# Performance work log

Hardware: AMD Instinct MI355X
Metric: run time of the kernel (lower is better)

## Reference

```python
import jax, jax.numpy as jnp
import numpy as np

EPS = 1e-6
H = 8          # num_heads
GAMMA = 0.99   # fixed decay (requires_grad=False in source)
RPE_LAYERS = 3


def srms(x):
    # SimpleRMSNorm: x / (rms(x) + eps), rms = ||x||_2 / sqrt(d) = sqrt(mean(x^2))
    return x / (jnp.sqrt(jnp.mean(x * x, axis=-1, keepdims=True)) + EPS)


def setup_inputs() -> dict:
    key = jax.random.key(0)
    B, N, E = 8, 2048, 512
    D1 = 1536            # int(3*512) // 8 * 8
    R = 512              # rpe_embedding
    ks = jax.random.split(key, 12)

    def lin(k, i, o):
        return jax.random.normal(k, (i, o), jnp.float32) * (i ** -0.5)

    x = jax.random.normal(ks[0], (B, N, E), jnp.float32)
    return {
        "x": x,
        "Wu": lin(ks[1], E, D1), "bu": jnp.zeros((D1,), jnp.float32),
        "Wv": lin(ks[2], E, D1), "bv": jnp.zeros((D1,), jnp.float32),
        "Wo": lin(ks[3], D1, E), "bo": jnp.zeros((E,), jnp.float32),
        "rpe_Win": lin(ks[4], 1, R), "rpe_bin": jnp.zeros((R,), jnp.float32),
        "rpe_W": jax.random.normal(ks[5], (RPE_LAYERS, R, R), jnp.float32) * (R ** -0.5),
        "rpe_b": jnp.zeros((RPE_LAYERS, R), jnp.float32),
        "rpe_Wout": lin(ks[6], R, D1), "rpe_bout": jnp.zeros((D1,), jnp.float32),
    }


def reference(x, Wu, bu, Wv, bv, Wo, bo, rpe_Win, rpe_bin, rpe_W, rpe_b, rpe_Wout, rpe_bout):
    B, N, E = x.shape
    u = jax.nn.silu(x @ Wu + bu)                     # b n d1
    v = jax.nn.silu(x @ Wv + bv)                     # b n d1
    D1 = v.shape[-1]
    D = D1 // H
    v = v.reshape(B, N, H, D).transpose(0, 2, 1, 3)  # b h n d

    # RPE MLP over positions: row 0 is the zero index, rows 1..N-1 are pos indices 1..N-1 (par_type=1)
    idx = jnp.arange(0, N, dtype=x.dtype)[:, None]   # (N, 1)
    h = idx @ rpe_Win + rpe_bin                      # (N, R)
    for i in range(RPE_LAYERS):                      # residual=False
        h = jax.nn.relu(srms(h)) @ rpe_W[i] + rpe_b[i]
    coeffs = jax.nn.relu(srms(h)) @ rpe_Wout + rpe_bout   # (N, H*D)
    coeffs = coeffs.reshape(N, H, D).transpose(1, 0, 2)   # h n d

    zero = coeffs[:, :1]                             # h 1 d  (a_0)
    pos = coeffs[:, 1:]                              # h n-1 d (a_1..a_{n-1})
    decay = GAMMA ** jnp.arange(1, N, dtype=x.dtype)[None, :, None]
    pos = pos * decay
    # causal: a = [a0, a1..a_{n-1}, a0]; act_type='none' -> identity
    a = jnp.concatenate([zero, pos, zero], axis=1)   # h, n+1, d

    # Toeplitz mixing via circular convolution of length 2n (torch.fft.rfft/irfft, norm='backward')
    m = 2 * N
    yf = jnp.fft.rfft(v, m, axis=2)                  # b h m/2+1 d (complex)
    af = jnp.fft.rfft(a, m, axis=1)[None]            # 1 h m/2+1 d
    out = jnp.fft.irfft(yf * af, m, axis=2)[:, :, :N, :]  # b h n d

    out = out.transpose(0, 2, 1, 3).reshape(B, N, D1)     # b n (h d)
    out = u * out
    return out @ Wo + bo
```

## Files before the change

### kernel.cpp

```cpp
#include <hip/hip_runtime.h>
#include <cstdint>


typedef unsigned short ushort_t;
typedef __attribute__((ext_vector_type(8))) short short8;
typedef __attribute__((ext_vector_type(4))) float f32x4;

#define AS1 __attribute__((address_space(1)))
#define AS3 __attribute__((address_space(3)))

#define SW1(j) ((j) ^ (((j) >> 4) & 15))
#define SW2(j) ((j) ^ ((((j) >> 6) & 7) << 1))

__device__ __forceinline__ float bf2f(ushort_t b) {
  union { unsigned u; float f; } x; x.u = ((unsigned)b) << 16; return x.f;
}
__device__ __forceinline__ ushort_t f2bf(float f) {
  union { float f; unsigned u; } x; x.f = f;
  unsigned r = x.u + 0x7fffu + ((x.u >> 16) & 1u);
  return (ushort_t)(r >> 16);
}

__device__ __forceinline__ void gload_lds16(const void* g, void* l) {
  auto gp = reinterpret_cast<const AS1 unsigned*>(reinterpret_cast<uintptr_t>(g));
  auto lp = reinterpret_cast<AS3 unsigned*>(reinterpret_cast<uintptr_t>(l));
  __builtin_amdgcn_global_load_lds(gp, lp, 16, 0, 0);
}

template<int MODE>
__launch_bounds__(256, 2)
__global__ void gemm_bt(const ushort_t* __restrict__ A, const ushort_t* __restrict__ Bt,
                        const float* __restrict__ bias, void* __restrict__ Cout,
                        void* __restrict__ Cout2, int M, int N, int K, float lng)
{
  __shared__ ushort_t As[128 * 64];
  __shared__ ushort_t Bs[128 * 64];
  const int tid  = threadIdx.x;
  const int wave = tid >> 6, lane = tid & 63;
  const int nb = N >> 7;
  const int bm = (int)blockIdx.x / nb, bn = (int)blockIdx.x % nb;
  const int m0 = bm << 7, n0 = bn << 7;
  const int lrow = lane & 15, quad = lane >> 4;
  const int wm = (wave >> 1) << 6, wn = (wave & 1) << 6;
  const int srow = lane >> 3;
  const int scol = (lane & 7) << 3;

  f32x4 acc[4][4] = {};

  for (int kt = 0; kt < K; kt += 64) {
    __syncthreads();
#pragma unroll
    for (int i = 0; i < 4; ++i) {
      const int ci  = i * 4 + wave;
      const int row = ci * 8 + srow;
      gload_lds16(A  + (long)(m0 + row) * K + kt + scol, (void*)&As[ci * 512]);
      gload_lds16(Bt + (long)(n0 + row) * K + kt + scol, (void*)&Bs[ci * 512]);
    }
    __syncthreads();
#pragma unroll
    for (int s = 0; s < 2; ++s) {
      short8 afr[4], bfr[4];
#pragma unroll
      for (int i = 0; i < 4; ++i)
        afr[i] = *(const short8*)&As[(wm + i * 16 + lrow) * 64 + s * 32 + quad * 8];
#pragma unroll
      for (int j = 0; j < 4; ++j)
        bfr[j] = *(const short8*)&Bs[(wn + j * 16 + lrow) * 64 + s * 32 + quad * 8];
#pragma unroll
      for (int i = 0; i < 4; ++i)
#pragma unroll
        for (int j = 0; j < 4; ++j)
          acc[i][j] = __builtin_amdgcn_mfma_f32_16x16x32_bf16(afr[i], bfr[j], acc[i][j], 0, 0, 0);
    }
  }

#pragma unroll
  for (int i = 0; i < 4; ++i) {
    const int rowb = m0 + wm + i * 16 + quad * 4;
#pragma unroll
    for (int j = 0; j < 4; ++j) {
      const int col = n0 + wn + j * 16 + lrow;
      const float bv = bias[col];
      if (MODE == 0) {
#pragma unroll
        for (int r = 0; r < 4; ++r)
          ((float*)Cout)[(long)(rowb + r) * N + col] = acc[i][j][r] + bv;
      } else {
        if (col < 1536) {
#pragma unroll
          for (int r = 0; r < 4; ++r) {
            float val = acc[i][j][r] + bv;
            float sv = val / (1.f + __expf(-val));
            ((ushort_t*)Cout)[(long)(rowb + r) * 1536 + col] = f2bf(sv);
          }
        } else {
          union { ushort_t h[4]; uint2 u2; } pk;
#pragma unroll
          for (int r = 0; r < 4; ++r) {
            float val = acc[i][j][r] + bv;
            float sv = val / (1.f + __expf(-val));
            pk.h[r] = f2bf(sv);
          }
          *(uint2*)((ushort_t*)Cout2 + (long)(col - 1536) * 16384 + rowb) = pk.u2;
        }
      }
    }
  }
}

template<int MODE>
__launch_bounds__(256, 2)
__global__ void gemm64_bt(const ushort_t* __restrict__ A, const ushort_t* __restrict__ Bt,
                          const float* __restrict__ bias, float* __restrict__ Cout,
                          int M, int N, int K, float lng)
{
  __shared__ ushort_t As[64 * 64];
  __shared__ ushort_t Bs[64 * 64];
  const int tid = threadIdx.x, wave = tid >> 6, lane = tid & 63;
  const int nb = N >> 6;
  const int bm = (int)blockIdx.x / nb, bn = (int)blockIdx.x % nb;
  const int m0 = bm << 6, n0 = bn << 6;
  const int lrow = lane & 15, quad = lane >> 4;
  const int wm = (wave >> 1) << 5, wn = (wave & 1) << 5;
  const int srow = lane >> 3, scol = (lane & 7) << 3;

  f32x4 acc[2][2] = {};

  for (int kt = 0; kt < K; kt += 64) {
    __syncthreads();
#pragma unroll
    for (int i = 0; i < 2; ++i) {
      const int ci = i * 4 + wave;
      const int row = ci * 8 + srow;
      gload_lds16(A  + (long)(m0 + row) * K + kt + scol, (void*)&As[ci * 512]);
      gload_lds16(Bt + (long)(n0 + row) * K + kt + scol, (void*)&Bs[ci * 512]);
    }
    __syncthreads();
#pragma unroll
    for (int s = 0; s < 2; ++s) {
      short8 afr[2], bfr[2];
#pragma unroll
      for (int i = 0; i < 2; ++i)
        afr[i] = *(const short8*)&As[(wm + i * 16 + lrow) * 64 + s * 32 + quad * 8];
#pragma unroll
      for (int j = 0; j < 2; ++j)
        bfr[j] = *(const short8*)&Bs[(wn + j * 16 + lrow) * 64 + s * 32 + quad * 8];
#pragma unroll
      for (int i = 0; i < 2; ++i)
#pragma unroll
        for (int j = 0; j < 2; ++j)
          acc[i][j] = __builtin_amdgcn_mfma_f32_16x16x32_bf16(afr[i], bfr[j], acc[i][j], 0, 0, 0);
    }
  }

#pragma unroll
  for (int i = 0; i < 2; ++i) {
    const int rowb = m0 + wm + i * 16 + quad * 4;
#pragma unroll
    for (int j = 0; j < 2; ++j) {
      const int col = n0 + wn + j * 16 + lrow;
      const float bv = bias[col];
#pragma unroll
      for (int r = 0; r < 4; ++r) {
        const int row = rowb + r;
        float val = acc[i][j][r] + bv;
        if (MODE == 0) Cout[(long)row * N + col] = val;
        else           Cout[(long)col * M + row] = val * __expf(lng * (float)row);
      }
    }
  }
}

__device__ __forceinline__ void srms_relu_store(float v0, float v1, ushort_t* out,
                                                long rowbase, int tid)
{
  float ss = v0 * v0 + v1 * v1;
#pragma unroll
  for (int off = 32; off; off >>= 1) ss += __shfl_down(ss, off);
  __shared__ float ps[4];
  const int wave = tid >> 6, lane = tid & 63;
  if (lane == 0) ps[wave] = ss;
  __syncthreads();
  float tot = ps[0] + ps[1] + ps[2] + ps[3];
  float sc = 1.f / (sqrtf(tot * (1.f / 512.f)) + 1e-6f);
  out[rowbase + tid]       = f2bf(fmaxf(v0 * sc, 0.f));
  out[rowbase + tid + 256] = f2bf(fmaxf(v1 * sc, 0.f));
}

__launch_bounds__(256)
__global__ void rpe_norm(const float* __restrict__ h, ushort_t* __restrict__ out)
{
  const int n = blockIdx.x, tid = threadIdx.x;
  float v0 = h[(long)n * 512 + tid];
  float v1 = h[(long)n * 512 + tid + 256];
  srms_relu_store(v0, v1, out, (long)n * 512, tid);
}

__device__ __forceinline__ void wtrans_body(const float* __restrict__ src,
                                            ushort_t* __restrict__ dst,
                                            int K, int N, int lb, int tid,
                                            float (*tile)[33])
{
  const int nbx = N >> 5;
  const int bx = lb % nbx, by = lb / nbx;
  const int n0 = bx << 5, k0 = by << 5;
  const int tx = tid & 31, ty = tid >> 5;
  for (int yy = ty; yy < 32; yy += 8)
    tile[yy][tx] = src[(long)(k0 + yy) * N + n0 + tx];
  __syncthreads();
  for (int yy = ty; yy < 32; yy += 8)
    dst[(long)(n0 + yy) * K + k0 + tx] = f2bf(tile[tx][yy]);
}

__launch_bounds__(256)
__global__ void prep_all(const float* __restrict__ Wu, const float* __restrict__ Wv,
                         const float* __restrict__ Wo, const float* __restrict__ rW,
                         const float* __restrict__ rWout,
                         const float* __restrict__ bu, const float* __restrict__ bv,
                         const float* __restrict__ x,
                         const float* __restrict__ rWin, const float* __restrict__ rbin,
                         ushort_t* __restrict__ wuvt, ushort_t* __restrict__ wot,
                         ushort_t* __restrict__ wrt, ushort_t* __restrict__ wroutt,
                         float* __restrict__ buvb, ushort_t* __restrict__ xb,
                         float2* __restrict__ twg, float2* __restrict__ twh,
                         ushort_t* __restrict__ a0)
{
  __shared__ float tile[32][33];
  const int bid = blockIdx.x, tid = threadIdx.x;
  if (bid < 3840) {
    const float* src; ushort_t* dst; int K, N, lb;
    if (bid < 768)       { src = Wu;    dst = wuvt;              K = 512;  N = 1536; lb = bid; }
    else if (bid < 1536) { src = Wv;    dst = wuvt + 1536L*512;  K = 512;  N = 1536; lb = bid - 768; }
    else if (bid < 2304) { src = Wo;    dst = wot;               K = 1536; N = 512;  lb = bid - 1536; }
    else if (bid < 2560) { src = rW;              dst = wrt;              K = 512; N = 512; lb = bid - 2304; }
    else if (bid < 2816) { src = rW + 512L*512;   dst = wrt + 512L*512;   K = 512; N = 512; lb = bid - 2560; }
    else if (bid < 3072) { src = rW + 2L*512*512; dst = wrt + 2L*512*512; K = 512; N = 512; lb = bid - 2816; }
    else                 { src = rWout; dst = wroutt;            K = 512;  N = 1536; lb = bid - 3072; }
    wtrans_body(src, dst, K, N, lb, tid, tile);
  } else if (bid < 3846) {
    int i = (bid - 3840) * 256 + tid;
    if (i < 1536) { buvb[i] = bu[i]; buvb[1536 + i] = bv[i]; }
  } else if (bid < 12038) {
    long i = (long)(bid - 3846) * 1024 + tid * 4;
    float4 f = *(const float4*)(x + i);
    unsigned lo = (unsigned)f2bf(f.x) | ((unsigned)f2bf(f.y) << 16);
    unsigned hi = (unsigned)f2bf(f.z) | ((unsigned)f2bf(f.w) << 16);
    *(uint2*)(xb + i) = make_uint2(lo, hi);
  } else if (bid < 12046) {
    int j = (bid - 12038) * 256 + tid;
    float s, c;
    __sincosf((float)j * (6.283185307179586f / 2048.f), &s, &c);
    twg[j] = make_float2(c, -s);
    float s2, c2;
    __sincosf((float)j * (3.14159265358979f / 2048.f), &s2, &c2);
    twh[j] = make_float2(c2, -s2);
  } else {
    const int n = bid - 12046;
    const float fn = (float)n;
    float v0 = fn * rWin[tid] + rbin[tid];
    float v1 = fn * rWin[tid + 256] + rbin[tid + 256];
    srms_relu_store(v0, v1, a0, (long)n * 512, tid);
  }
}

__device__ __forceinline__ float2 cmulf(float2 a, float2 b) {
  return make_float2(a.x * b.x - a.y * b.y, a.x * b.y + a.y * b.x);
}
__device__ __forceinline__ float2 cadd(float2 a, float2 b){ return make_float2(a.x+b.x, a.y+b.y); }
__device__ __forceinline__ float2 csub(float2 a, float2 b){ return make_float2(a.x-b.x, a.y-b.y); }
__device__ __forceinline__ float2 cmni(float2 z){ return make_float2(z.y, -z.x); }
__device__ __forceinline__ float2 cw8(float2 z){
  const float s = 0.70710678118654752f;
  return make_float2(s*(z.x+z.y), s*(z.y-z.x));
}
__device__ __forceinline__ float2 cw83(float2 z){
  const float s = 0.70710678118654752f;
  return make_float2(s*(z.y-z.x), -s*(z.x+z.y));
}

__device__ __forceinline__ void dft8(const float2* u, float2* y)
{
  float2 a0=cadd(u[0],u[4]), a1=cadd(u[1],u[5]), a2=cadd(u[2],u[6]), a3=cadd(u[3],u[7]);
  float2 b0=csub(u[0],u[4]), b1=cw8(csub(u[1],u[5])), b2=cmni(csub(u[2],u[6])), b3=cw83(csub(u[3],u[7]));
  float2 c0=cadd(a0,a2), c1=csub(a0,a2), c2=cadd(a1,a3), c3=cmni(csub(a1,a3));
  y[0]=cadd(c0,c2); y[2]=cadd(c1,c3); y[4]=csub(c0,c2); y[6]=csub(c1,c3);
  float2 d0=cadd(b0,b2), d1=csub(b0,b2), d2=cadd(b1,b3), d3=cmni(csub(b1,b3));
  y[1]=cadd(d0,d2); y[3]=cadd(d1,d3); y[5]=csub(d0,d2); y[7]=csub(d1,d3);
}
__device__ __forceinline__ void dft8_hz(const float2* u, float2* y)
{
  float2 b1=cw8(u[1]), b2=cmni(u[2]), b3=cw83(u[3]);
  float2 c0=cadd(u[0],u[2]), c1=csub(u[0],u[2]), c2=cadd(u[1],u[3]), c3=cmni(csub(u[1],u[3]));
  y[0]=cadd(c0,c2); y[2]=cadd(c1,c3); y[4]=csub(c0,c2); y[6]=csub(c1,c3);
  float2 d0=cadd(u[0],b2), d1=csub(u[0],b2), d2=cadd(b1,b3), d3=cmni(csub(b1,b3));
  y[1]=cadd(d0,d2); y[3]=cadd(d1,d3); y[5]=csub(d0,d2); y[7]=csub(d1,d3);
}

template<bool HZ>
__device__ void fft2048_r8_2(float2* b0a, float2* b1a, float2* b0b, float2* b1b,
                             const float2* __restrict__ tw, int tid)
{
  float2 u[8], v[8], y[8], z[8];
  {
    const int i = tid;
#pragma unroll
    for (int m = 0; m < (HZ ? 4 : 8); ++m) { u[m] = b0a[i + 256*m]; v[m] = b0b[i + 256*m]; }
    if (HZ) { dft8_hz(u, y); dft8_hz(v, z); } else { dft8(u, y); dft8(v, z); }
    const int j = i << 3;
#pragma unroll
    for (int m = 0; m < 8; ++m) { b1a[SW1(j + m)] = y[m]; b1b[SW1(j + m)] = z[m]; }
  }
  __syncthreads();
  {
    const int i = tid, k = i & 7, tb = k << 5;
    float2 w[8];
#pragma unroll
    for (int m = 1; m < 8; ++m) w[m] = tw[m * tb];
#pragma unroll
    for (int m = 0; m < 8; ++m) { u[m] = b1a[SW1(i + 256*m)]; v[m] = b1b[SW1(i + 256*m)]; }
#pragma unroll
    for (int m = 1; m < 8; ++m) { u[m] = cmulf(u[m], w[m]); v[m] = cmulf(v[m], w[m]); }
    dft8(u, y); dft8(v, z);
    const int j = ((i - k) << 3) + k;
#pragma unroll
    for (int m = 0; m < 8; ++m) { b0a[SW2(j + 8*m)] = y[m]; b0b[SW2(j + 8*m)] = z[m]; }
  }
  __syncthreads();
  {
    const int i = tid, k = i & 63, tb = k << 2;
    float2 w[8];
#pragma unroll
    for (int m = 1; m < 8; ++m) w[m] = tw[m * tb];
#pragma unroll
    for (int m = 0; m < 8; ++m) { u[m] = b0a[SW2(i + 256*m)]; v[m] = b0b[SW2(i + 256*m)]; }
#pragma unroll
    for (int m = 1; m < 8; ++m) { u[m] = cmulf(u[m], w[m]); v[m] = cmulf(v[m], w[m]); }
    dft8(u, y); dft8(v, z);
    const int j = ((i - k) << 3) + k;
#pragma unroll
    for (int m = 0; m < 8; ++m) { b1a[j + 64*m] = y[m]; b1b[j + 64*m] = z[m]; }
  }
  __syncthreads();
#pragma unroll
  for (int hh = 0; hh < 2; ++hh) {
    const int i = tid + (hh << 8);
    float2 w1 = tw[i], w2 = tw[2 * i], w3 = tw[3 * i];
    float2 q0 = b1a[i], q1 = b1a[i + 512], q2 = b1a[i + 1024], q3 = b1a[i + 1536];
    float2 r0 = b1b[i], r1 = b1b[i + 512], r2 = b1b[i + 1024], r3 = b1b[i + 1536];
    q1 = cmulf(q1, w1); q2 = cmulf(q2, w2); q3 = cmulf(q3, w3);
    r1 = cmulf(r1, w1); r2 = cmulf(r2, w2); r3 = cmulf(r3, w3);
    {
      float2 v0 = cadd(q0, q2), v2 = csub(q0, q2);
      float2 v1 = cadd(q1, q3), v3 = cmni(csub(q1, q3));
      b0a[i]        = cadd(v0, v1);
      b0a[i + 512]  = cadd(v2, v3);
      b0a[i + 1024] = csub(v0, v1);
      b0a[i + 1536] = csub(v2, v3);
    }
    {
      float2 v0 = cadd(r0, r2), v2 = csub(r0, r2);
      float2 v1 = cadd(r1, r3), v3 = cmni(csub(r1, r3));
      b0b[i]        = cadd(v0, v1);
      b0b[i + 512]  = cadd(v2, v3);
      b0b[i + 1024] = csub(v0, v1);
      b0b[i + 1536] = csub(v2, v3);
    }
  }
  __syncthreads();
}

__launch_bounds__(256, 2)
__global__ void fft_kernel_spec(const float* __restrict__ kern, float2* __restrict__ af,
                                const float2* __restrict__ twg, const float2* __restrict__ twh)
{
  __shared__ float2 bx0[2048], by0[2048], bx1[2048], by1[2048];
  const int tid = threadIdx.x;
  const int c0 = (int)blockIdx.x * 2;
  const float* ka = kern + (long)c0 * 2048;
  const float* kb = ka + 2048;
  for (int j = tid; j < 1024; j += 256) {
    bx0[j] = *(const float2*)(ka + 2 * j);
    bx1[j] = *(const float2*)(kb + 2 * j);
  }
  __syncthreads();
  fft2048_r8_2<true>(bx0, by0, bx1, by1, twg, tid);
  float2* af0 = af + (long)c0 * 2052;
  float2* af1 = af0 + 2052;
  for (int k = tid; k <= 1024; k += 256) {
    const float2 W = twh[k];
    const int kn = (2048 - k) & 2047;
    {
      float2 Zk = bx0[k], Zn = bx0[kn];
      float2 E = make_float2(0.5f * (Zk.x + Zn.x), 0.5f * (Zk.y - Zn.y));
      float2 O = make_float2(0.5f * (Zk.y + Zn.y), 0.5f * (Zn.x - Zk.x));
      float2 WO = cmulf(W, O);
      af0[k] = make_float2(E.x + WO.x, E.y + WO.y);
      if (k != 0 && k != 1024) af0[2048 - k] = make_float2(E.x - WO.x, -(E.y - WO.y));
      if (k == 0)              af0[2048]     = make_float2(E.x - WO.x, -(E.y - WO.y));
    }
    {
      float2 Zk = bx1[k], Zn = bx1[kn];
      float2 E = make_float2(0.5f * (Zk.x + Zn.x), 0.5f * (Zk.y - Zn.y));
      float2 O = make_float2(0.5f * (Zk.y + Zn.y), 0.5f * (Zn.x - Zk.x));
      float2 WO = cmulf(W, O);
      af1[k] = make_float2(E.x + WO.x, E.y + WO.y);
      if (k != 0 && k != 1024) af1[2048 - k] = make_float2(E.x - WO.x, -(E.y - WO.y));
      if (k == 0)              af1[2048]     = make_float2(E.x - WO.x, -(E.y - WO.y));
    }
  }
}

__launch_bounds__(256, 2)
__global__ void fft_conv(ushort_t* __restrict__ vt, const float2* __restrict__ af,
                         const float2* __restrict__ twg, const float2* __restrict__ twh)
{
  __shared__ float2 bx0[2048], by0[2048], bx1[2048], by1[2048];
  const int tid = threadIdx.x;
  const long s0 = (long)blockIdx.x * 2;
  const int c = (int)(s0 >> 3);
  ushort_t* vsa = vt + s0 * 2048;
  ushort_t* vsb = vsa + 2048;
#pragma unroll
  for (int jj = 0; jj < 4; ++jj) {
    const int j = tid + jj * 256;
    unsigned pa = *(const unsigned*)(vsa + 2 * j);
    unsigned pb = *(const unsigned*)(vsb + 2 * j);
    bx0[j] = make_float2(bf2f((ushort_t)(pa & 0xffffu)), bf2f((ushort_t)(pa >> 16)));
    bx1[j] = make_float2(bf2f((ushort_t)(pb & 0xffffu)), bf2f((ushort_t)(pb >> 16)));
  }
  __syncthreads();
  fft2048_r8_2<true>(bx0, by0, bx1, by1, twg, tid);
  const float2* afc = af + (long)c * 2052;
  for (int k = tid; k <= 1024; k += 256) {
    const float2 A0 = afc[k], A1 = afc[2048 - k], W = twh[k];
    const float2 cW = make_float2(W.x, -W.y);
    const int kn = (2048 - k) & 2047;
    {
      float2 Zk = bx0[k], Zn = bx0[kn];
      float2 E = make_float2(0.5f * (Zk.x + Zn.x), 0.5f * (Zk.y - Zn.y));
      float2 O = make_float2(0.5f * (Zk.y + Zn.y), 0.5f * (Zn.x - Zk.x));
      float2 WO = cmulf(W, O);
      float2 Xk = make_float2(E.x + WO.x, E.y + WO.y);
      float2 Xn = make_float2(E.x - WO.x, -(E.y - WO.y));
      float2 Pk = cmulf(Xk, A0);
      float2 Pn = cmulf(Xn, A1);
      float2 E2 = make_float2(0.5f * (Pk.x + Pn.x), 0.5f * (Pk.y - Pn.y));
      float2 G  = make_float2(0.5f * (Pk.x - Pn.x), 0.5f * (Pk.y + Pn.y));
      float2 Fo = cmulf(cW, G);
      by0[k] = make_float2(E2.x - Fo.y, -(E2.y + Fo.x));
      if (k != 0 && k != 1024)
        by0[2048 - k] = make_float2(E2.x + Fo.y, E2.y - Fo.x);
    }
    {
      float2 Zk = bx1[k], Zn = bx1[kn];
      float2 E = make_float2(0.5f * (Zk.x + Zn.x), 0.5f * (Zk.y - Zn.y));
      float2 O = make_float2(0.5f * (Zk.y + Zn.y), 0.5f * (Zn.x - Zk.x));
      float2 WO = cmulf(W, O);
      float2 Xk = make_float2(E.x + WO.x, E.y + WO.y);
      float2 Xn = make_float2(E.x - WO.x, -(E.y - WO.y));
      float2 Pk = cmulf(Xk, A0);
      float2 Pn = cmulf(Xn, A1);
      float2 E2 = make_float2(0.5f * (Pk.x + Pn.x), 0.5f * (Pk.y - Pn.y));
      float2 G  = make_float2(0.5f * (Pk.x - Pn.x), 0.5f * (Pk.y + Pn.y));
      float2 Fo = cmulf(cW, G);
      by1[k] = make_float2(E2.x - Fo.y, -(E2.y + Fo.x));
      if (k != 0 && k != 1024)
        by1[2048 - k] = make_float2(E2.x + Fo.y, E2.y - Fo.x);
    }
  }
  __syncthreads();
  fft2048_r8_2<false>(by0, bx0, by1, bx1, twg, tid);
  const float inv = 1.f / 2048.f;
#pragma unroll
  for (int jj = 0; jj < 4; ++jj) {
    const int j = tid + jj * 256;
    float2 ra = by0[j], rb = by1[j];
    unsigned oa = (unsigned)f2bf(ra.x * inv) | ((unsigned)f2bf(-ra.y * inv) << 16);
    unsigned ob = (unsigned)f2bf(rb.x * inv) | ((unsigned)f2bf(-rb.y * inv) << 16);
    *(unsigned*)(vsa + 2 * j) = oa;
    *(unsigned*)(vsb + 2 * j) = ob;
  }
}

__launch_bounds__(256)
__global__ void gate_trans(const ushort_t* __restrict__ convt, ushort_t* __restrict__ u)
{
  __shared__ ushort_t tile[64][65];
  const int bc = (int)blockIdx.x % 24, br = (int)blockIdx.x / 24;
  const int c0 = bc << 6, r0 = br << 6;
  const int tx = threadIdx.x & 63, ty = threadIdx.x >> 6;
  for (int yy = ty; yy < 64; yy += 4)
    tile[yy][tx] = convt[(long)(c0 + yy) * 16384 + r0 + tx];
  __syncthreads();
  for (int yy = ty; yy < 64; yy += 4) {
    long ui = (long)(r0 + yy) * 1536 + c0 + tx;
    float uu = bf2f(u[ui]);
    float cc = bf2f(tile[tx][yy]);
    u[ui] = f2bf(uu * cc);
  }
}

extern "C" void kernel_launch(void* const* d_in, const int* in_sizes, int n_in,
                              void* d_out, int out_size, void* d_ws, size_t ws_size,
                              hipStream_t stream)
{
  const float* x     = (const float*)d_in[0];
  const float* Wu    = (const float*)d_in[1];
  const float* bu    = (const float*)d_in[2];
  const float* Wv    = (const float*)d_in[3];
  const float* bv    = (const float*)d_in[4];
  const float* Wo    = (const float*)d_in[5];
  const float* bo    = (const float*)d_in[6];
  const float* rWin  = (const float*)d_in[7];
  const float* rbin  = (const float*)d_in[8];
  const float* rW    = (const float*)d_in[9];
  const float* rb    = (const float*)d_in[10];
  const float* rWout = (const float*)d_in[11];
  const float* rbout = (const float*)d_in[12];

  char* base = (char*)d_ws;
  size_t off = 0;
  auto alloc = [&](size_t bytes) -> char* {
    size_t r = (off + 255) & ~(size_t)255; off = r + bytes; return base + r;
  };
  ushort_t* wuvt   = (ushort_t*)alloc(3072L * 512 * 2);
  ushort_t* wot    = (ushort_t*)alloc(512L * 1536 * 2);
  ushort_t* wrt    = (ushort_t*)alloc(3L * 512 * 512 * 2);
  ushort_t* wroutt = (ushort_t*)alloc(1536L * 512 * 2);
  float*    buvb   = (float*)   alloc(3072L * 4);
  ushort_t* a0     = (ushort_t*)alloc(2048L * 512 * 2);
  float2*   af     = (float2*)  alloc(1536L * 2052 * 8);
  float2*   twg    = (float2*)  alloc(2048L * 8);
  float2*   twh    = (float2*)  alloc(2048L * 8);
  char*     X      = alloc(16384L * 512 * 2);
  ushort_t* u      = (ushort_t*)alloc(16384L * 1536 * 2);
  ushort_t* vt     = (ushort_t*)alloc(1536L * 16384 * 2);
  ushort_t* xb   = (ushort_t*)X;
  float*    h    = (float*)X;
  float*    kern = (float*)(X + 4L * 1024 * 1024);

  const float lng = -0.01005033585350145f;

  prep_all<<<dim3(14094), dim3(256), 0, stream>>>(
      Wu, Wv, Wo, rW, rWout, bu, bv, x, rWin, rbin,
      wuvt, wot, wrt, wroutt, buvb, xb, twg, twh, a0);

  gemm_bt<3><<<dim3(3072), dim3(256), 0, stream>>>(xb, wuvt, buvb, u, vt,
                                                   16384, 3072, 512, 0.f);

  for (int i = 0; i < 3; ++i) {
    gemm64_bt<0><<<dim3(256), dim3(256), 0, stream>>>(a0, wrt + (long)i * 512 * 512,
                                                      rb + (long)i * 512, h,
                                                      2048, 512, 512, 0.f);
    rpe_norm<<<dim3(2048), dim3(256), 0, stream>>>(h, a0);
  }
  gemm64_bt<2><<<dim3(768), dim3(256), 0, stream>>>(a0, wroutt, rbout, kern,
                                                    2048, 1536, 512, lng);
  fft_kernel_spec<<<dim3(768), dim3(256), 0, stream>>>(kern, af, twg, twh);

  fft_conv<<<dim3(6144), dim3(256), 0, stream>>>(vt, af, twg, twh);
  gate_trans<<<dim3(6144), dim3(256), 0, stream>>>(vt, u);
  gemm_bt<0><<<dim3(512), dim3(256), 0, stream>>>(u, wot, bo, d_out, nullptr,
                                                  16384, 512, 1536, 0.f);
}
```

Baseline: 493.8 us.

## Make the 2048-point FFT in-place to halve LDS and double occupancy

Replaces the ping-pong shared-memory FFT, which used four 2048-entry float2 buffers, with an in-place variant that uses two buffers. A barrier is added after each stage's loads so results can be written back into the same buffer. The spectral multiply in the convolution kernel now also writes in place. The LDS cut lets launch bounds rise from 2 to 4 blocks per CU, aiming to hide LDS and global latency in the FFT kernels, at the cost of extra barriers and a tighter per-thread register budget that could cause spills.

```diff
diff --git a/kernel.cpp b/kernel.cpp
--- a/kernel.cpp
+++ b/kernel.cpp
@@ -297,18 +297,19 @@
 }
 
 template<bool HZ>
-__device__ void fft2048_r8_2(float2* b0a, float2* b1a, float2* b0b, float2* b1b,
-                             const float2* __restrict__ tw, int tid)
+__device__ void fft2048_ip2(float2* ba, float2* bb,
+                            const float2* __restrict__ tw, int tid)
 {
   float2 u[8], v[8], y[8], z[8];
   {
     const int i = tid;
 #pragma unroll
-    for (int m = 0; m < (HZ ? 4 : 8); ++m) { u[m] = b0a[i + 256*m]; v[m] = b0b[i + 256*m]; }
+    for (int m = 0; m < (HZ ? 4 : 8); ++m) { u[m] = ba[i + 256*m]; v[m] = bb[i + 256*m]; }
     if (HZ) { dft8_hz(u, y); dft8_hz(v, z); } else { dft8(u, y); dft8(v, z); }
+    __syncthreads();
     const int j = i << 3;
 #pragma unroll
-    for (int m = 0; m < 8; ++m) { b1a[SW1(j + m)] = y[m]; b1b[SW1(j + m)] = z[m]; }
+    for (int m = 0; m < 8; ++m) { ba[SW1(j + m)] = y[m]; bb[SW1(j + m)] = z[m]; }
   }
   __syncthreads();
   {
@@ -317,13 +318,14 @@
 #pragma unroll
     for (int m = 1; m < 8; ++m) w[m] = tw[m * tb];
 #pragma unroll
-    for (int m = 0; m < 8; ++m) { u[m] = b1a[SW1(i + 256*m)]; v[m] = b1b[SW1(i + 256*m)]; }
+    for (int m = 0; m < 8; ++m) { u[m] = ba[SW1(i + 256*m)]; v[m] = bb[SW1(i + 256*m)]; }
 #pragma unroll
     for (int m = 1; m < 8; ++m) { u[m] = cmulf(u[m], w[m]); v[m] = cmulf(v[m], w[m]); }
     dft8(u, y); dft8(v, z);
+    __syncthreads();
     const int j = ((i - k) << 3) + k;
 #pragma unroll
-    for (int m = 0; m < 8; ++m) { b0a[SW2(j + 8*m)] = y[m]; b0b[SW2(j + 8*m)] = z[m]; }
+    for (int m = 0; m < 8; ++m) { ba[SW2(j + 8*m)] = y[m]; bb[SW2(j + 8*m)] = z[m]; }
   }
   __syncthreads();
   {
@@ -332,48 +334,49 @@
 #pragma unroll
     for (int m = 1; m < 8; ++m) w[m] = tw[m * tb];
 #pragma unroll
-    for (int m = 0; m < 8; ++m) { u[m] = b0a[SW2(i + 256*m)]; v[m] = b0b[SW2(i + 256*m)]; }
+    for (int m = 0; m < 8; ++m) { u[m] = ba[SW2(i + 256*m)]; v[m] = bb[SW2(i + 256*m)]; }
 #pragma unroll
     for (int m = 1; m < 8; ++m) { u[m] = cmulf(u[m], w[m]); v[m] = cmulf(v[m], w[m]); }
     dft8(u, y); dft8(v, z);
+    __syncthreads();
     const int j = ((i - k) << 3) + k;
 #pragma unroll
-    for (int m = 0; m < 8; ++m) { b1a[j + 64*m] = y[m]; b1b[j + 64*m] = z[m]; }
+    for (int m = 0; m < 8; ++m) { ba[j + 64*m] = y[m]; bb[j + 64*m] = z[m]; }
   }
   __syncthreads();
 #pragma unroll
   for (int hh = 0; hh < 2; ++hh) {
     const int i = tid + (hh << 8);
     float2 w1 = tw[i], w2 = tw[2 * i], w3 = tw[3 * i];
-    float2 q0 = b1a[i], q1 = b1a[i + 512], q2 = b1a[i + 1024], q3 = b1a[i + 1536];
-    float2 r0 = b1b[i], r1 = b1b[i + 512], r2 = b1b[i + 1024], r3 = b1b[i + 1536];
+    float2 q0 = ba[i], q1 = ba[i + 512], q2 = ba[i + 1024], q3 = ba[i + 1536];
+    float2 r0 = bb[i], r1 = bb[i + 512], r2 = bb[i + 1024], r3 = bb[i + 1536];
     q1 = cmulf(q1, w1); q2 = cmulf(q2, w2); q3 = cmulf(q3, w3);
     r1 = cmulf(r1, w1); r2 = cmulf(r2, w2); r3 = cmulf(r3, w3);
     {
       float2 v0 = cadd(q0, q2), v2 = csub(q0, q2);
       float2 v1 = cadd(q1, q3), v3 = cmni(csub(q1, q3));
-      b0a[i]        = cadd(v0, v1);
-      b0a[i + 512]  = cadd(v2, v3);
-      b0a[i + 1024] = csub(v0, v1);
-      b0a[i + 1536] = csub(v2, v3);
+      ba[i]        = cadd(v0, v1);
+      ba[i + 512]  = cadd(v2, v3);
+      ba[i + 1024] = csub(v0, v1);
+      ba[i + 1536] = csub(v2, v3);
     }
     {
       float2 v0 = cadd(r0, r2), v2 = csub(r0, r2);
       float2 v1 = cadd(r1, r3), v3 = cmni(csub(r1, r3));
-      b0b[i]        = cadd(v0, v1);
-      b0b[i + 512]  = cadd(v2, v3);
-      b0b[i + 1024] = csub(v0, v1);
-      b0b[i + 1536] = csub(v2, v3);
-    }
-  }
-  __syncthreads();
-}
-
-__launch_bounds__(256, 2)
+      bb[i]        = cadd(v0, v1);
+      bb[i + 512]  = cadd(v2, v3);
+      bb[i + 1024] = csub(v0, v1);
+      bb[i + 1536] = csub(v2, v3);
+    }
+  }
+  __syncthreads();
+}
+
+__launch_bounds__(256, 4)
 __global__ void fft_kernel_spec(const float* __restrict__ kern, float2* __restrict__ af,
                                 const float2* __restrict__ twg, const float2* __restrict__ twh)
 {
-  __shared__ float2 bx0[2048], by0[2048], bx1[2048], by1[2048];
+  __shared__ float2 bx0[2048], bx1[2048];
   const int tid = threadIdx.x;
   const int c0 = (int)blockIdx.x * 2;
   const float* ka = kern + (long)c0 * 2048;
@@ -383,7 +386,7 @@
     bx1[j] = *(const float2*)(kb + 2 * j);
   }
   __syncthreads();
-  fft2048_r8_2<true>(bx0, by0, bx1, by1, twg, tid);
+  fft2048_ip2<true>(bx0, bx1, twg, tid);
   float2* af0 = af + (long)c0 * 2052;
   float2* af1 = af0 + 2052;
   for (int k = tid; k <= 1024; k += 256) {
@@ -410,11 +413,11 @@
   }
 }
 
-__launch_bounds__(256, 2)
+__launch_bounds__(256, 4)
 __global__ void fft_conv(ushort_t* __restrict__ vt, const float2* __restrict__ af,
                          const float2* __restrict__ twg, const float2* __restrict__ twh)
 {
-  __shared__ float2 bx0[2048], by0[2048], bx1[2048], by1[2048];
+  __shared__ float2 bx0[2048], bx1[2048];
   const int tid = threadIdx.x;
   const long s0 = (long)blockIdx.x * 2;
   const int c = (int)(s0 >> 3);
@@ -429,7 +432,7 @@
     bx1[j] = make_float2(bf2f((ushort_t)(pb & 0xffffu)), bf2f((ushort_t)(pb >> 16)));
   }
   __syncthreads();
-  fft2048_r8_2<true>(bx0, by0, bx1, by1, twg, tid);
+  fft2048_ip2<true>(bx0, bx1, twg, tid);
   const float2* afc = af + (long)c * 2052;
   for (int k = tid; k <= 1024; k += 256) {
     const float2 A0 = afc[k], A1 = afc[2048 - k], W = twh[k];
@@ -447,9 +450,9 @@
       float2 E2 = make_float2(0.5f * (Pk.x + Pn.x), 0.5f * (Pk.y - Pn.y));
       float2 G  = make_float2(0.5f * (Pk.x - Pn.x), 0.5f * (Pk.y + Pn.y));
       float2 Fo = cmulf(cW, G);
-      by0[k] = make_float2(E2.x - Fo.y, -(E2.y + Fo.x));
+      bx0[k] = make_float2(E2.x - Fo.y, -(E2.y + Fo.x));
       if (k != 0 && k != 1024)
-        by0[2048 - k] = make_float2(E2.x + Fo.y, E2.y - Fo.x);
+        bx0[2048 - k] = make_float2(E2.x + Fo.y, E2.y - Fo.x);
     }
     {
       float2 Zk = bx1[k], Zn = bx1[kn];
@@ -463,18 +466,18 @@
       float2 E2 = make_float2(0.5f * (Pk.x + Pn.x), 0.5f * (Pk.y - Pn.y));
       float2 G  = make_float2(0.5f * (Pk.x - Pn.x), 0.5f * (Pk.y + Pn.y));
       float2 Fo = cmulf(cW, G);
-      by1[k] = make_float2(E2.x - Fo.y, -(E2.y + Fo.x));
+      bx1[k] = make_float2(E2.x - Fo.y, -(E2.y + Fo.x));
       if (k != 0 && k != 1024)
-        by1[2048 - k] = make_float2(E2.x + Fo.y, E2.y - Fo.x);
-    }
-  }
-  __syncthreads();
-  fft2048_r8_2<false>(by0, bx0, by1, bx1, twg, tid);
+        bx1[2048 - k] = make_float2(E2.x + Fo.y, E2.y - Fo.x);
+    }
+  }
+  __syncthreads();
+  fft2048_ip2<false>(bx0, bx1, twg, tid);
   const float inv = 1.f / 2048.f;
 #pragma unroll
   for (int jj = 0; jj < 4; ++jj) {
     const int j = tid + jj * 256;
-    float2 ra = by0[j], rb = by1[j];
+    float2 ra = bx0[j], rb = bx1[j];
     unsigned oa = (unsigned)f2bf(ra.x * inv) | ((unsigned)f2bf(-ra.y * inv) << 16);
     unsigned ob = (unsigned)f2bf(rb.x * inv) | ((unsigned)f2bf(-rb.y * inv) << 16);
     *(unsigned*)(vsa + 2 * j) = oa;
```

Result: faster. 457.0 us (-7.5%).
